# Kernel optimization log

Hardware: AMD Instinct MI355X
Metric: run time of the kernel (lower is better)

The kernel has to match this reference:

```python
import jax, jax.numpy as jnp
import numpy as np

EPS = 1e-12  # F.normalize default eps

def _l2_normalize(v):
    # torch.nn.functional.normalize: v / max(||v||_2, eps)
    n = jnp.sqrt(jnp.sum(v * v, axis=-1, keepdims=True))
    return v / jnp.maximum(n, EPS)

def setup_inputs() -> dict:
    key = jax.random.key(0)
    k1, k2 = jax.random.split(key)
    B, M, D = 4096, 12893, 2048
    x = jax.random.normal(k1, (B, D), dtype=jnp.float32)
    prototypes = jax.random.normal(k2, (M, D), dtype=jnp.float32)
    distance_scale = jnp.ones((1,), dtype=jnp.float32)
    return {"x": x, "prototypes": prototypes, "distance_scale": distance_scale}

def reference(x, prototypes, distance_scale):
    xn = _l2_normalize(x)            # [B, D]
    pn = _l2_normalize(prototypes)   # [M, D]
    # pairwise Euclidean distance via ||a||^2 + ||b||^2 - 2 a.b (stable clamp)
    xs = jnp.sum(xn * xn, axis=-1, keepdims=True)        # [B, 1]
    ps = jnp.sum(pn * pn, axis=-1)[None, :]              # [1, M]
    d2 = xs + ps - 2.0 * jnp.einsum('bd,md->bm', xn, pn)  # [B, M]
    dist = jnp.sqrt(jnp.maximum(d2, 0.0))
    x3 = -jnp.abs(distance_scale[0]) * dist              # [B, M]
    # original forward returns (x3, x3, x3, x3); all identical
    return x3
```

## Files before the change

### kernel.cpp

```cpp
#include <hip/hip_runtime.h>
#include <hip/hip_bf16.h>
#include <cstdint>
#include <cstddef>

constexpr int BROWS = 4096;
constexpr int MREAL = 12893;
constexpr int MPAD  = 12928;
constexpr int KDIM  = 2048;
constexpr int NT    = KDIM / 64;

typedef __attribute__((ext_vector_type(8))) short short8;
typedef __attribute__((ext_vector_type(4))) float f32x4;

__device__ __forceinline__ void gld_lds16(const void* g, void* l) {
  __builtin_amdgcn_global_load_lds((__attribute__((address_space(1))) const void*)g,
                                   (__attribute__((address_space(3))) void*)l,
                                   16, 0, 0);
}

__global__ void l2norm_fused(const float* __restrict__ x,
                             const float* __restrict__ p,
                             __hip_bfloat16* __restrict__ xn,
                             __hip_bfloat16* __restrict__ pn) {
  const int b = blockIdx.x;
  const int t = threadIdx.x;
  const float* irow;
  __hip_bfloat16* orow;
  if (b < BROWS) {
    irow = x + (size_t)b * KDIM;
    orow = xn + (size_t)b * KDIM;
  } else {
    const int row = b - BROWS;
    orow = pn + (size_t)row * KDIM;
    if (row >= MREAL) {
      reinterpret_cast<float4*>(orow)[t] = make_float4(0.f, 0.f, 0.f, 0.f);
      return;
    }
    irow = p + (size_t)row * KDIM;
  }

  const float4* iv = reinterpret_cast<const float4*>(irow);
  float4 a = iv[t];
  float4 c = iv[t + 256];
  float ss = a.x*a.x + a.y*a.y + a.z*a.z + a.w*a.w
           + c.x*c.x + c.y*c.y + c.z*c.z + c.w*c.w;

  #pragma unroll
  for (int off = 32; off > 0; off >>= 1) ss += __shfl_down(ss, off);

  __shared__ float red[4];
  if ((t & 63) == 0) red[t >> 6] = ss;
  __syncthreads();
  float tot = red[0] + red[1] + red[2] + red[3];
  float inv = 1.0f / fmaxf(sqrtf(tot), 1e-12f);

  union { ushort4 u; __hip_bfloat16 h[4]; } o1, o2;
  o1.h[0] = __float2bfloat16(a.x * inv);
  o1.h[1] = __float2bfloat16(a.y * inv);
  o1.h[2] = __float2bfloat16(a.z * inv);
  o1.h[3] = __float2bfloat16(a.w * inv);
  o2.h[0] = __float2bfloat16(c.x * inv);
  o2.h[1] = __float2bfloat16(c.y * inv);
  o2.h[2] = __float2bfloat16(c.z * inv);
  o2.h[3] = __float2bfloat16(c.w * inv);
  reinterpret_cast<ushort4*>(orow)[t]       = o1.u;
  reinterpret_cast<ushort4*>(orow)[t + 256] = o2.u;
}

__global__ __launch_bounds__(512, 2)
void gemm_dist(const __hip_bfloat16* __restrict__ A,
               const __hip_bfloat16* __restrict__ P,
               const float* __restrict__ scale,
               float* __restrict__ out) {
  __shared__ __hip_bfloat16 lds[65536];
  __hip_bfloat16* const sA = lds;
  __hip_bfloat16* const sB = lds + 32768;

  const int t    = threadIdx.x;
  const int lane = t & 63;
  const int wv   = t >> 6;
  const int wm   = wv >> 2;
  const int wn   = wv & 3;

  const int bid = blockIdx.x;
  const int swz = (bid & 7) * 102 + (bid >> 3);
  const int bm0 = (swz / 51) * 256;
  const int bn0 = (swz % 51) * 256;

  const int srow = t >> 3;
  const int sp   = t & 7;
  const int ssl  = sp ^ (srow & 7);
  const __hip_bfloat16* aSrc[4];
  const __hip_bfloat16* bSrc[4];
  int sOff[4];
  #pragma unroll
  for (int r = 0; r < 4; ++r) {
    aSrc[r] = A + (size_t)(bm0 + r*64 + srow) * KDIM + ssl*8;
    int br = bn0 + r*64 + srow;
    br = br < MPAD ? br : (MPAD - 1);
    bSrc[r] = P + (size_t)br * KDIM + ssl*8;
    sOff[r] = (r*64 + srow)*64 + sp*8;
  }

  const int l15 = lane & 15, hi = lane >> 4;
  const int pk0 = ( hi      ^ (lane & 7)) * 8;
  const int pk1 = ((hi + 4) ^ (lane & 7)) * 8;
  const int aBase = (wm*128 + l15) * 64;
  const int bBase = (wn*64  + l15) * 64;

  f32x4 acc[8][4];
  #pragma unroll
  for (int i = 0; i < 8; ++i)
    #pragma unroll
    for (int j = 0; j < 4; ++j) acc[i][j] = f32x4{0.f, 0.f, 0.f, 0.f};

#define STG_A(BUF, R, T) do { const int kt_ = ((T)*64) & (KDIM-1);            \
    gld_lds16(aSrc[(R)]   + kt_, sA + (BUF)*16384 + sOff[(R)]);               \
    gld_lds16(aSrc[(R)+1] + kt_, sA + (BUF)*16384 + sOff[(R)+1]); } while(0)
#define STG_B(BUF, R, T) do { const int kt_ = ((T)*64) & (KDIM-1);            \
    gld_lds16(bSrc[(R)]   + kt_, sB + (BUF)*16384 + sOff[(R)]);               \
    gld_lds16(bSrc[(R)+1] + kt_, sB + (BUF)*16384 + sOff[(R)+1]); } while(0)

  STG_A(0, 0, 0); STG_A(0, 2, 0);
  STG_B(0, 0, 0); STG_B(0, 2, 0);
  STG_B(1, 0, 1); STG_B(1, 2, 1);
  asm volatile("s_waitcnt vmcnt(4)" ::: "memory");
  __builtin_amdgcn_s_barrier();

  short8 bfr[4][2];

#define PHASE(BUF, Q, READB, STG, VM) do {                                    \
    asm volatile("" ::: "memory");                                            \
    const __hip_bfloat16* sAb = sA + (BUF)*16384;                             \
    const __hip_bfloat16* sBb = sB + (BUF)*16384;                             \
    if (READB) {                                                              \
      _Pragma("unroll")                                                       \
      for (int j = 0; j < 4; ++j) {                                           \
        bfr[j][0] = *reinterpret_cast<const short8*>(sBb + bBase + j*1024 + pk0); \
        bfr[j][1] = *reinterpret_cast<const short8*>(sBb + bBase + j*1024 + pk1); \
      }                                                                       \
    }                                                                         \
    const short8 a00 = *reinterpret_cast<const short8*>(sAb + aBase + (Q)*2048 + pk0); \
    const short8 a01 = *reinterpret_cast<const short8*>(sAb + aBase + (Q)*2048 + pk1); \
    const short8 a10 = *reinterpret_cast<const short8*>(sAb + aBase + (Q)*2048 + 1024 + pk0); \
    const short8 a11 = *reinterpret_cast<const short8*>(sAb + aBase + (Q)*2048 + 1024 + pk1); \
    STG;                                                                      \
    __builtin_amdgcn_s_barrier();                                             \
    asm volatile("s_waitcnt lgkmcnt(0)" ::: "memory");                        \
    __builtin_amdgcn_s_setprio(1);                                            \
    _Pragma("unroll")                                                         \
    for (int j = 0; j < 4; ++j) {                                             \
      acc[2*(Q)  ][j] = __builtin_amdgcn_mfma_f32_16x16x32_bf16(a00, bfr[j][0], acc[2*(Q)  ][j], 0, 0, 0); \
      acc[2*(Q)  ][j] = __builtin_amdgcn_mfma_f32_16x16x32_bf16(a01, bfr[j][1], acc[2*(Q)  ][j], 0, 0, 0); \
      acc[2*(Q)+1][j] = __builtin_amdgcn_mfma_f32_16x16x32_bf16(a10, bfr[j][0], acc[2*(Q)+1][j], 0, 0, 0); \
      acc[2*(Q)+1][j] = __builtin_amdgcn_mfma_f32_16x16x32_bf16(a11, bfr[j][1], acc[2*(Q)+1][j], 0, 0, 0); \
    }                                                                         \
    __builtin_amdgcn_s_setprio(0);                                            \
    if (VM) asm volatile("s_waitcnt vmcnt(4)" ::: "memory");                  \
    __builtin_amdgcn_s_barrier();                                             \
  } while (0)

  for (int it = 0; it < NT/2; ++it) {
    const int T1 = 2*it + 1;
    PHASE(0, 0, true , STG_A(1, 0, T1),     false);
    PHASE(0, 1, false, STG_A(1, 2, T1),     false);
    PHASE(0, 2, false, STG_B(0, 0, (T1+1)), false);
    PHASE(0, 3, false, STG_B(0, 2, (T1+1)), true );
    PHASE(1, 0, true , STG_A(0, 0, (T1+1)), false);
    PHASE(1, 1, false, STG_A(0, 2, (T1+1)), false);
    PHASE(1, 2, false, STG_B(1, 0, (T1+2)), false);
    PHASE(1, 3, false, STG_B(1, 2, (T1+2)), true );
  }

  const float s = fabsf(scale[0]);
  const int colb = bn0 + wn*64 + l15;
  #pragma unroll
  for (int i = 0; i < 8; ++i) {
    const int rowb = bm0 + wm*128 + i*16 + hi*4;
    #pragma unroll
    for (int j = 0; j < 4; ++j) {
      const int col = colb + j*16;
      if (col < MREAL) {
        #pragma unroll
        for (int r = 0; r < 4; ++r) {
          float d2 = fmaxf(2.0f - 2.0f*acc[i][j][r], 0.0f);
          out[(size_t)(rowb + r)*MREAL + col] = -s * __builtin_sqrtf(d2);
        }
      }
    }
  }
  asm volatile("s_waitcnt vmcnt(0)" ::: "memory");
}

#undef PHASE
#undef STG_A
#undef STG_B

extern "C" void kernel_launch(void* const* d_in, const int* in_sizes, int n_in,
                              void* d_out, int out_size, void* d_ws, size_t ws_size,
                              hipStream_t stream) {
  const float* x = (const float*)d_in[0];
  const float* p = (const float*)d_in[1];
  const float* s = (const float*)d_in[2];
  float* out = (float*)d_out;

  __hip_bfloat16* xn = (__hip_bfloat16*)d_ws;
  __hip_bfloat16* pn = xn + (size_t)BROWS * KDIM;

  l2norm_fused<<<BROWS + MPAD, 256, 0, stream>>>(x, p, xn, pn);

  gemm_dist<<<816, 512, 0, stream>>>(xn, pn, s, out);
}
```

Baseline: 522.6 us.

## Use one wave per row in l2norm and deepen GEMM global-to-LDS prefetch

The normalization kernel now assigns one 64-lane wave per row and reduces with xor shuffles. This removes the shared-memory reduction and the block barrier. The GEMM staging schedule is reordered so that A-tile row pairs for the next K step are issued earlier. The vmcnt waits are relaxed from 4 to 6 outstanding loads, and an lgkmcnt wait is added when B fragments are read. Together these aim to keep more global loads in flight across the MFMA phases, at the cost of a more delicate ordering between loads and barriers that could expose races or stalls.

```diff
diff --git a/kernel.cpp b/kernel.cpp
--- a/kernel.cpp
+++ b/kernel.cpp
@@ -22,49 +22,51 @@
                              const float* __restrict__ p,
                              __hip_bfloat16* __restrict__ xn,
                              __hip_bfloat16* __restrict__ pn) {
-  const int b = blockIdx.x;
-  const int t = threadIdx.x;
+  const int wid  = (int)((blockIdx.x * (unsigned)blockDim.x + threadIdx.x) >> 6);
+  const int lane = threadIdx.x & 63;
+
   const float* irow;
   __hip_bfloat16* orow;
-  if (b < BROWS) {
-    irow = x + (size_t)b * KDIM;
-    orow = xn + (size_t)b * KDIM;
+  if (wid < BROWS) {
+    irow = x + (size_t)wid * KDIM;
+    orow = xn + (size_t)wid * KDIM;
   } else {
-    const int row = b - BROWS;
+    const int row = wid - BROWS;
     orow = pn + (size_t)row * KDIM;
     if (row >= MREAL) {
-      reinterpret_cast<float4*>(orow)[t] = make_float4(0.f, 0.f, 0.f, 0.f);
+      ushort4 z = {0, 0, 0, 0};
+      #pragma unroll
+      for (int j = 0; j < 8; ++j)
+        reinterpret_cast<ushort4*>(orow)[lane + 64 * j] = z;
       return;
     }
     irow = p + (size_t)row * KDIM;
   }
 
   const float4* iv = reinterpret_cast<const float4*>(irow);
-  float4 a = iv[t];
-  float4 c = iv[t + 256];
-  float ss = a.x*a.x + a.y*a.y + a.z*a.z + a.w*a.w
-           + c.x*c.x + c.y*c.y + c.z*c.z + c.w*c.w;
-
-  #pragma unroll
-  for (int off = 32; off > 0; off >>= 1) ss += __shfl_down(ss, off);
-
-  __shared__ float red[4];
-  if ((t & 63) == 0) red[t >> 6] = ss;
-  __syncthreads();
-  float tot = red[0] + red[1] + red[2] + red[3];
-  float inv = 1.0f / fmaxf(sqrtf(tot), 1e-12f);
-
-  union { ushort4 u; __hip_bfloat16 h[4]; } o1, o2;
-  o1.h[0] = __float2bfloat16(a.x * inv);
-  o1.h[1] = __float2bfloat16(a.y * inv);
-  o1.h[2] = __float2bfloat16(a.z * inv);
-  o1.h[3] = __float2bfloat16(a.w * inv);
-  o2.h[0] = __float2bfloat16(c.x * inv);
-  o2.h[1] = __float2bfloat16(c.y * inv);
-  o2.h[2] = __float2bfloat16(c.z * inv);
-  o2.h[3] = __float2bfloat16(c.w * inv);
-  reinterpret_cast<ushort4*>(orow)[t]       = o1.u;
-  reinterpret_cast<ushort4*>(orow)[t + 256] = o2.u;
+  float4 v[8];
+  #pragma unroll
+  for (int j = 0; j < 8; ++j) v[j] = iv[lane + 64 * j];
+
+  float ss = 0.f;
+  #pragma unroll
+  for (int j = 0; j < 8; ++j)
+    ss += v[j].x * v[j].x + v[j].y * v[j].y + v[j].z * v[j].z + v[j].w * v[j].w;
+
+  #pragma unroll
+  for (int off = 1; off < 64; off <<= 1) ss += __shfl_xor(ss, off);
+
+  const float inv = 1.0f / fmaxf(sqrtf(ss), 1e-12f);
+
+  #pragma unroll
+  for (int j = 0; j < 8; ++j) {
+    union { ushort4 u; __hip_bfloat16 h[4]; } o;
+    o.h[0] = __float2bfloat16(v[j].x * inv);
+    o.h[1] = __float2bfloat16(v[j].y * inv);
+    o.h[2] = __float2bfloat16(v[j].z * inv);
+    o.h[3] = __float2bfloat16(v[j].w * inv);
+    reinterpret_cast<ushort4*>(orow)[lane + 64 * j] = o.u;
+  }
 }
 
 __global__ __launch_bounds__(512, 2)
@@ -114,17 +116,18 @@
     #pragma unroll
     for (int j = 0; j < 4; ++j) acc[i][j] = f32x4{0.f, 0.f, 0.f, 0.f};
 
-#define STG_A(BUF, R, T) do { const int kt_ = ((T)*64) & (KDIM-1);            \
-    gld_lds16(aSrc[(R)]   + kt_, sA + (BUF)*16384 + sOff[(R)]);               \
-    gld_lds16(aSrc[(R)+1] + kt_, sA + (BUF)*16384 + sOff[(R)+1]); } while(0)
-#define STG_B(BUF, R, T) do { const int kt_ = ((T)*64) & (KDIM-1);            \
-    gld_lds16(bSrc[(R)]   + kt_, sB + (BUF)*16384 + sOff[(R)]);               \
-    gld_lds16(bSrc[(R)+1] + kt_, sB + (BUF)*16384 + sOff[(R)+1]); } while(0)
-
-  STG_A(0, 0, 0); STG_A(0, 2, 0);
-  STG_B(0, 0, 0); STG_B(0, 2, 0);
-  STG_B(1, 0, 1); STG_B(1, 2, 1);
-  asm volatile("s_waitcnt vmcnt(4)" ::: "memory");
+#define STG_AP(BUF, Ra, Rb, T) do { const int kt_ = ((T)*64) & (KDIM-1);      \
+    gld_lds16(aSrc[(Ra)] + kt_, sA + (BUF)*16384 + sOff[(Ra)]);               \
+    gld_lds16(aSrc[(Rb)] + kt_, sA + (BUF)*16384 + sOff[(Rb)]); } while(0)
+#define STG_BP(BUF, Ra, Rb, T) do { const int kt_ = ((T)*64) & (KDIM-1);      \
+    gld_lds16(bSrc[(Ra)] + kt_, sB + (BUF)*16384 + sOff[(Ra)]);               \
+    gld_lds16(bSrc[(Rb)] + kt_, sB + (BUF)*16384 + sOff[(Rb)]); } while(0)
+
+  STG_BP(0, 0, 1, 0); STG_BP(0, 2, 3, 0);
+  STG_AP(0, 0, 2, 0); STG_AP(0, 1, 3, 0);
+  STG_BP(1, 0, 1, 1); STG_BP(1, 2, 3, 1);
+  STG_AP(1, 0, 2, 1);
+  asm volatile("s_waitcnt vmcnt(6)" ::: "memory");
   __builtin_amdgcn_s_barrier();
 
   short8 bfr[4][2];
@@ -145,6 +148,7 @@
     const short8 a10 = *reinterpret_cast<const short8*>(sAb + aBase + (Q)*2048 + 1024 + pk0); \
     const short8 a11 = *reinterpret_cast<const short8*>(sAb + aBase + (Q)*2048 + 1024 + pk1); \
     STG;                                                                      \
+    if (READB) asm volatile("s_waitcnt lgkmcnt(8)" ::: "memory");             \
     __builtin_amdgcn_s_barrier();                                             \
     asm volatile("s_waitcnt lgkmcnt(0)" ::: "memory");                        \
     __builtin_amdgcn_s_setprio(1);                                            \
@@ -156,20 +160,20 @@
       acc[2*(Q)+1][j] = __builtin_amdgcn_mfma_f32_16x16x32_bf16(a11, bfr[j][1], acc[2*(Q)+1][j], 0, 0, 0); \
     }                                                                         \
     __builtin_amdgcn_s_setprio(0);                                            \
-    if (VM) asm volatile("s_waitcnt vmcnt(4)" ::: "memory");                  \
+    if (VM) asm volatile("s_waitcnt vmcnt(6)" ::: "memory");                  \
     __builtin_amdgcn_s_barrier();                                             \
   } while (0)
 
   for (int it = 0; it < NT/2; ++it) {
-    const int T1 = 2*it + 1;
-    PHASE(0, 0, true , STG_A(1, 0, T1),     false);
-    PHASE(0, 1, false, STG_A(1, 2, T1),     false);
-    PHASE(0, 2, false, STG_B(0, 0, (T1+1)), false);
-    PHASE(0, 3, false, STG_B(0, 2, (T1+1)), true );
-    PHASE(1, 0, true , STG_A(0, 0, (T1+1)), false);
-    PHASE(1, 1, false, STG_A(0, 2, (T1+1)), false);
-    PHASE(1, 2, false, STG_B(1, 0, (T1+2)), false);
-    PHASE(1, 3, false, STG_B(1, 2, (T1+2)), true );
+    const int T0 = 2*it, T1 = 2*it + 1;
+    PHASE(0, 0, true , STG_AP(1, 1, 3, T1),                            false);
+    PHASE(0, 1, false, STG_BP(0, 0, 1, (T0+2)),                        false);
+    PHASE(0, 2, false, { STG_BP(0, 2, 3, (T0+2)); STG_AP(0, 0, 2, (T0+2)); }, false);
+    PHASE(0, 3, false, {  },                           true );
+    PHASE(1, 0, true , STG_AP(0, 1, 3, (T0+2)),                        false);
+    PHASE(1, 1, false, STG_BP(1, 0, 1, (T1+2)),                        false);
+    PHASE(1, 2, false, { STG_BP(1, 2, 3, (T1+2)); STG_AP(1, 0, 2, (T1+2)); }, false);
+    PHASE(1, 3, false, {  },                           true );
   }
 
   const float s = fabsf(scale[0]);
@@ -193,8 +197,8 @@
 }
 
 #undef PHASE
-#undef STG_A
-#undef STG_B
+#undef STG_AP
+#undef STG_BP
 
 extern "C" void kernel_launch(void* const* d_in, const int* in_sizes, int n_in,
                               void* d_out, int out_size, void* d_ws, size_t ws_size,
@@ -207,7 +211,7 @@
   __hip_bfloat16* xn = (__hip_bfloat16*)d_ws;
   __hip_bfloat16* pn = xn + (size_t)BROWS * KDIM;
 
-  l2norm_fused<<<BROWS + MPAD, 256, 0, stream>>>(x, p, xn, pn);
+  l2norm_fused<<<(BROWS + MPAD) / 4, 256, 0, stream>>>(x, p, xn, pn);
 
   gemm_dist<<<816, 512, 0, stream>>>(xn, pn, s, out);
 }
```

Result: no change. 531.8 us (+1.8%).
